# Performance work log

Hardware: AMD Instinct MI355X
Metric: run time of the kernel (lower is better)

The kernel has to match this reference:

```python
import jax, jax.numpy as jnp
import numpy as np

DM = 1024      # dmodel
HQK = 1024     # heads*dq == heads*dk == heads*dv
FF = 4096
VOCAB = 32000
NCAT = 75
DK = 64        # per-head dk used for 1/sqrt(dk) scaling
UNK_IDX = 1
EPS = 1e-5


def pos_encoding(n, dm):
    pos = jnp.arange(n, dtype=jnp.float32)[:, None]                  # [n,1]
    power = jnp.arange(0, dm, 2, dtype=jnp.float32) / dm             # [dm/2]
    denom = jnp.power(10000.0, power)                                # [dm/2]
    ang = pos / denom                                                # [n,dm/2]
    # even cols = sin, odd cols = cos (interleaved)
    return jnp.stack([jnp.sin(ang), jnp.cos(ang)], axis=-1).reshape(n, dm)


def layernorm(x, g, b):
    mu = jnp.mean(x, axis=-1, keepdims=True)
    var = jnp.var(x, axis=-1, keepdims=True)
    return (x - mu) * jax.lax.rsqrt(var + EPS) * g + b


def setup_inputs() -> dict:
    key = jax.random.key(0)
    ks = jax.random.split(key, 16)
    s = 0.02
    inp = {
        "input_indices": jax.random.randint(ks[0], (8, 2048), 0, VOCAB),
        "emb": jax.random.normal(ks[1], (VOCAB, DM), jnp.float32) * s,
        "Wq": jax.random.normal(ks[2], (DM, HQK), jnp.float32) * s,
        "bq": jnp.zeros((HQK,), jnp.float32),
        "Wk": jax.random.normal(ks[3], (DM, HQK), jnp.float32) * s,
        "bk": jnp.zeros((HQK,), jnp.float32),
        "Wv": jax.random.normal(ks[4], (DM, HQK), jnp.float32) * s,
        "bv": jnp.zeros((HQK,), jnp.float32),
        "Wu": jax.random.normal(ks[5], (HQK, DM), jnp.float32) * s,
        "bu": jnp.zeros((DM,), jnp.float32),
        "g1": jnp.ones((DM,), jnp.float32),
        "be1": jnp.zeros((DM,), jnp.float32),
        "W1": jax.random.normal(ks[6], (DM, FF), jnp.float32) * s,
        "b1": jnp.zeros((FF,), jnp.float32),
        "W2": jax.random.normal(ks[7], (FF, DM), jnp.float32) * s,
        "b2": jnp.zeros((DM,), jnp.float32),
        "g2": jnp.ones((DM,), jnp.float32),
        "be2": jnp.zeros((DM,), jnp.float32),
        "W3": jax.random.normal(ks[8], (DM, DM // 2), jnp.float32) * s,
        "b3": jnp.zeros((DM // 2,), jnp.float32),
        "W4": jax.random.normal(ks[9], (DM // 2, NCAT), jnp.float32) * s,
        "b4": jnp.zeros((NCAT,), jnp.float32),
        "g3": jnp.ones((NCAT,), jnp.float32),
        "be3": jnp.zeros((NCAT,), jnp.float32),
    }
    return inp


def reference(input_indices, emb, Wq, bq, Wk, bk, Wv, bv, Wu, bu, g1, be1,
              W1, b1, W2, b2, g2, be2, W3, b3, W4, b4, g3, be3):
    d, n = input_indices.shape
    idx = jnp.where(input_indices >= VOCAB, UNK_IDX, input_indices)
    x = emb[idx] + pos_encoding(n, DM)[None]                          # [d,n,dm]
    # attention WITHOUT softmax: scores = QK^T/sqrt(dk); attn = scores @ V
    q = x @ Wq + bq
    k = x @ Wk + bk
    v = x @ Wv + bv
    scores = jnp.einsum('bnd,bmd->bnm', q, k) / (DK ** 0.5)           # [d,n,n]
    attn = jnp.einsum('bnm,bmd->bnd', scores, v)                      # [d,n,hdv]
    u = attn @ Wu + bu
    h1 = layernorm(x + u, g1, be1)
    ffo = jax.nn.relu(h1 @ W1 + b1) @ W2 + b2
    h2 = layernorm(h1 + ffo, g2, be2)
    logits = jax.nn.relu(h2 @ W3 + b3) @ W4 + b4                      # [d,n,75]
    return jax.nn.sigmoid(layernorm(logits, g3, be3))
```

## Files before the change

### kernel.cpp

```cpp
#include <hip/hip_runtime.h>
#include <hip/hip_fp16.h>
#include <math.h>

#define DM    1024
#define FFD   4096
#define VOCAB 32000
#define NCAT  75
#define UNK_IDX 1
#define EPS   1e-5f
#define NB    8
#define SEQ   2048
#define T_TOK (NB*SEQ)

using u16   = unsigned short;
using half_t = _Float16;
using half8 = __attribute__((ext_vector_type(8))) _Float16;
using f32x4 = __attribute__((ext_vector_type(4))) float;

struct alignas(8) h4 { half_t s[4]; };

__device__ __forceinline__ void async16(const half_t* g, half_t* l) {
    __builtin_amdgcn_global_load_lds(
        (const __attribute__((address_space(1))) void*)g,
        (__attribute__((address_space(3))) void*)l,
        16, 0, 0);
}

__global__ __launch_bounds__(256)
void pe_kernel(float* __restrict__ pe)
{
    int gid = blockIdx.x * blockDim.x + threadIdx.x;
    if (gid >= SEQ * DM) return;
    int dcol = gid & (DM - 1);
    int t    = gid >> 10;
    int p = dcol >> 1;
    float power = (float)p / 512.0f;
    float denom = powf(10000.0f, power);
    float ang = (float)t / denom;
    pe[gid] = (dcol & 1) ? cosf(ang) : sinf(ang);
}

__global__ __launch_bounds__(256)
void embed_pos_kernel(const int* __restrict__ idx,
                      const float* __restrict__ emb,
                      const float* __restrict__ pe,
                      float* __restrict__ xf, half_t* __restrict__ xh)
{
    int gid4 = blockIdx.x * blockDim.x + threadIdx.x;
    if (gid4 >= T_TOK * DM / 4) return;
    int tok = gid4 >> 8;
    int c4  = (gid4 & 255) << 2;
    int t   = tok & (SEQ - 1);
    int id = idx[tok];
    if (id >= VOCAB || id < 0) id = UNK_IDX;
    float4 e = *(const float4*)(emb + (long long)id * DM + c4);
    float4 q = *(const float4*)(pe + (long long)t * DM + c4);
    float4 v = make_float4(e.x + q.x, e.y + q.y, e.z + q.z, e.w + q.w);
    *(float4*)(xf + (long long)tok * DM + c4) = v;
    h4 pk = {{(half_t)v.x, (half_t)v.y, (half_t)v.z, (half_t)v.w}};
    *(h4*)(xh + (long long)tok * DM + c4) = pk;
}

__global__ __launch_bounds__(256)
void transpose_h_kernel(const float* __restrict__ in, half_t* __restrict__ out,
                        int K, int N, int Npad)
{
    __shared__ float t[32][33];
    int n0 = blockIdx.x * 32, k0 = blockIdx.y * 32;
    int tx = threadIdx.x & 31, ty = threadIdx.x >> 5;
#pragma unroll
    for (int i = 0; i < 4; i++) {
        int k = k0 + ty + i * 8, n = n0 + tx;
        t[ty + i * 8][tx] = (k < K && n < N) ? in[(long long)k * N + n] : 0.f;
    }
    __syncthreads();
#pragma unroll
    for (int i = 0; i < 4; i++) {
        int n = n0 + ty + i * 8, k = k0 + tx;
        if (n < Npad && k < K)
            out[(long long)n * K + k] = (half_t)t[tx][ty + i * 8];
    }
}

__global__ __launch_bounds__(128)
void pad_bias_kernel(const float* __restrict__ b, float* __restrict__ bp)
{
    int i = threadIdx.x;
    bp[i] = (i < NCAT) ? b[i] : 0.f;
}

template<int OUT_MODE>
__global__ __launch_bounds__(256)
void gemm_nt(const half_t* __restrict__ A, const half_t* __restrict__ B,
             const float* __restrict__ bias, const float* __restrict__ resid,
             void* __restrict__ Cout,
             int M, int N, int K, int ld,
             long long sA, long long sB, long long sC,
             float scale, int do_relu)
{
    A += (long long)blockIdx.z * sA;
    B += (long long)blockIdx.z * sB;
    const int tid  = threadIdx.x;
    const int lane = tid & 63;
    const int w    = tid >> 6;
    const int wm   = w >> 1, wn = w & 1;
    const long long row0 = (long long)blockIdx.y * 128;
    const long long col0 = (long long)blockIdx.x * 128;

    __shared__ half_t smem[4 * 4096];
    half_t* const As = smem;
    half_t* const Bs = smem + 2 * 4096;

    f32x4 acc[4][4];
    const f32x4 zero = {0.f, 0.f, 0.f, 0.f};
#pragma unroll
    for (int i = 0; i < 4; i++)
#pragma unroll
        for (int j = 0; j < 4; j++) acc[i][j] = zero;

    const int ldrow = lane >> 2;
    const int swcol = (((lane & 3) << 3)) ^ ((ldrow & 3) << 3);
    const int fr    = lane & 15;
    const int kk8   = (lane >> 4) << 3;

    const int KT = K / 32;

#define ISSUE(k0, buf)                                                         \
    {                                                                          \
        _Pragma("unroll")                                                      \
        for (int it = 0; it < 2; ++it) {                                       \
            int rb = (it * 4 + w) * 16;                                        \
            long long ao = (row0 + rb + ldrow) * (long long)ld + (k0) + swcol; \
            long long bo = (col0 + rb + ldrow) * (long long)ld + (k0) + swcol; \
            async16(A + ao, As + (buf) * 4096 + rb * 32);                      \
            async16(B + bo, Bs + (buf) * 4096 + rb * 32);                      \
        }                                                                      \
    }

    ISSUE(0, 0);
    for (int kt = 0; kt < KT; ++kt) {
        const int cur = kt & 1;
        __syncthreads();
        if (kt + 1 < KT) ISSUE((kt + 1) * 32, cur ^ 1);

        half8 af[4], bf[4];
#pragma unroll
        for (int i = 0; i < 4; ++i) {
            int r   = wm * 64 + i * 16 + fr;
            int off = cur * 4096 + r * 32 + (kk8 ^ ((r & 3) << 3));
            af[i] = *(const half8*)(As + off);
        }
#pragma unroll
        for (int j = 0; j < 4; ++j) {
            int r   = wn * 64 + j * 16 + fr;
            int off = cur * 4096 + r * 32 + (kk8 ^ ((r & 3) << 3));
            bf[j] = *(const half8*)(Bs + off);
        }
#pragma unroll
        for (int i = 0; i < 4; ++i)
#pragma unroll
            for (int j = 0; j < 4; ++j)
                acc[i][j] = __builtin_amdgcn_mfma_f32_16x16x32_f16(
                    af[i], bf[j], acc[i][j], 0, 0, 0);
    }
#undef ISSUE

    float* ls = (float*)smem;
    const int ldp = 132;
    const int qr = (lane >> 4) * 4;
    const int lc = lane & 15;
    float bvj[4];
#pragma unroll
    for (int j = 0; j < 4; ++j)
        bvj[j] = bias ? bias[col0 + wn * 64 + j * 16 + lc] : 0.f;
    const float* rz = (OUT_MODE == 0 && resid) ? resid + (long long)blockIdx.z * sC : nullptr;

#pragma unroll
    for (int i = 0; i < 4; ++i) {
        __syncthreads();
#pragma unroll
        for (int j = 0; j < 4; ++j) {
            int col = wn * 64 + j * 16 + lc;
#pragma unroll
            for (int r = 0; r < 4; ++r) {
                float f = acc[i][j][r] * scale + bvj[j];
                if (do_relu) f = fmaxf(f, 0.f);
                ls[(wm * 16 + qr + r) * ldp + col] = f;
            }
        }
        __syncthreads();
        if (OUT_MODE == 2) {
#pragma unroll
            for (int rep = 0; rep < 4; ++rep) {
                int idx = rep * 256 + tid;
                int n   = idx >> 3;
                int k   = idx & 7;
                int lr0 = k * 4;
                h4 pk;
                long long arow0 = (lr0 < 16 ? 0 : 48) + i * 16 + lr0;
#pragma unroll
                for (int r = 0; r < 4; ++r)
                    pk.s[r] = (half_t)ls[(lr0 + r) * ldp + n];
                long long gr = row0 + arow0;
                int b  = (int)(gr >> 11);
                int tl = (int)(gr & (SEQ - 1));
                half_t* C = (half_t*)Cout;
                *(h4*)(C + (long long)b * N * SEQ + (col0 + n) * SEQ + tl) = pk;
            }
        } else {
#pragma unroll
            for (int rep = 0; rep < 4; ++rep) {
                int idx = rep * 256 + tid;
                int lr  = idx >> 5;
                int c4  = (idx & 31) << 2;
                long long arow = (lr < 16 ? 0 : 48) + i * 16 + lr;
                float4 v = *(float4*)&ls[lr * ldp + c4];
                long long base = (row0 + arow) * N + col0 + c4;
                if (OUT_MODE == 0) {
                    float* C = (float*)Cout + blockIdx.z * sC;
                    if (rz) {
                        float4 x = *(const float4*)(rz + base);
                        v.x += x.x; v.y += x.y; v.z += x.z; v.w += x.w;
                    }
                    *(float4*)(C + base) = v;
                } else {
                    half_t* C = (half_t*)Cout + blockIdx.z * sC;
                    h4 pk = {{(half_t)v.x, (half_t)v.y, (half_t)v.z, (half_t)v.w}};
                    *(h4*)(C + base) = pk;
                }
            }
        }
    }
}

__global__ __launch_bounds__(256)
void add_ln_kernel(const float* __restrict__ X, const float* __restrict__ Y,
                   const float* __restrict__ g, const float* __restrict__ b,
                   float* __restrict__ outf, half_t* __restrict__ outh)
{
    int row = blockIdx.x;
    int tid = threadIdx.x;
    float4 v = ((const float4*)(X + (long long)row * DM))[tid];
    if (Y) {
        float4 y = ((const float4*)(Y + (long long)row * DM))[tid];
        v.x += y.x; v.y += y.y; v.z += y.z; v.w += y.w;
    }
    float s  = v.x + v.y + v.z + v.w;
    float s2 = v.x * v.x + v.y * v.y + v.z * v.z + v.w * v.w;
#pragma unroll
    for (int o = 1; o < 64; o <<= 1) {
        s  += __shfl_xor(s,  o, 64);
        s2 += __shfl_xor(s2, o, 64);
    }
    __shared__ float rs[4], rs2[4], stats[2];
    int wid = tid >> 6;
    if ((tid & 63) == 0) { rs[wid] = s; rs2[wid] = s2; }
    __syncthreads();
    if (tid == 0) {
        float S  = rs[0] + rs[1] + rs[2] + rs[3];
        float S2 = rs2[0] + rs2[1] + rs2[2] + rs2[3];
        float mean = S / (float)DM;
        float var  = S2 / (float)DM - mean * mean;
        stats[0] = mean;
        stats[1] = rsqrtf(var + EPS);
    }
    __syncthreads();
    float mean = stats[0], rstd = stats[1];
    float4 gg = ((const float4*)g)[tid];
    float4 bb = ((const float4*)b)[tid];
    float4 o;
    o.x = (v.x - mean) * rstd * gg.x + bb.x;
    o.y = (v.y - mean) * rstd * gg.y + bb.y;
    o.z = (v.z - mean) * rstd * gg.z + bb.z;
    o.w = (v.w - mean) * rstd * gg.w + bb.w;
    if (outf) ((float4*)(outf + (long long)row * DM))[tid] = o;
    h4 pk = {{(half_t)o.x, (half_t)o.y, (half_t)o.z, (half_t)o.w}};
    *(h4*)(outh + (long long)row * DM + tid * 4) = pk;
}

__global__ __launch_bounds__(64)
void ln75_sigmoid_kernel(const float* __restrict__ L,
                         const float* __restrict__ g, const float* __restrict__ b,
                         float* __restrict__ out)
{
    int row = blockIdx.x;
    int t   = threadIdx.x;
    const float* lr = L + (long long)row * 128;
    float e0 = (t < NCAT) ? lr[t] : 0.f;
    float e1 = (t + 64 < NCAT) ? lr[t + 64] : 0.f;
    float s  = e0 + e1;
    float s2 = e0 * e0 + e1 * e1;
#pragma unroll
    for (int o = 1; o < 64; o <<= 1) {
        s  += __shfl_xor(s,  o, 64);
        s2 += __shfl_xor(s2, o, 64);
    }
    float mean = s / (float)NCAT;
    float var  = s2 / (float)NCAT - mean * mean;
    float rstd = rsqrtf(var + EPS);
    if (t < NCAT) {
        float z = (e0 - mean) * rstd * g[t] + b[t];
        out[(long long)row * NCAT + t] = 1.f / (1.f + expf(-z));
    }
    if (t + 64 < NCAT) {
        float z = (e1 - mean) * rstd * g[t + 64] + b[t + 64];
        out[(long long)row * NCAT + t + 64] = 1.f / (1.f + expf(-z));
    }
}

extern "C" void kernel_launch(void* const* d_in, const int* in_sizes, int n_in,
                              void* d_out, int out_size, void* d_ws, size_t ws_size,
                              hipStream_t stream)
{
    const int*   idx = (const int*)  d_in[0];
    const float* emb = (const float*)d_in[1];
    const float* Wq  = (const float*)d_in[2];
    const float* bq  = (const float*)d_in[3];
    const float* Wk  = (const float*)d_in[4];
    const float* bk  = (const float*)d_in[5];
    const float* Wv  = (const float*)d_in[6];
    const float* bv  = (const float*)d_in[7];
    const float* Wu  = (const float*)d_in[8];
    const float* bu  = (const float*)d_in[9];
    const float* g1  = (const float*)d_in[10];
    const float* be1 = (const float*)d_in[11];
    const float* W1  = (const float*)d_in[12];
    const float* b1  = (const float*)d_in[13];
    const float* W2  = (const float*)d_in[14];
    const float* b2  = (const float*)d_in[15];
    const float* g2  = (const float*)d_in[16];
    const float* be2 = (const float*)d_in[17];
    const float* W3  = (const float*)d_in[18];
    const float* b3  = (const float*)d_in[19];
    const float* W4  = (const float*)d_in[20];
    const float* b4  = (const float*)d_in[21];
    const float* g3  = (const float*)d_in[22];
    const float* be3 = (const float*)d_in[23];

    const long long TD  = (long long)T_TOK * DM;
    char* p = (char*)d_ws;
    char* R_A = p; p += TD * 4;
    char* R_B = p; p += TD * 2;
    char* R_C = p; p += TD * 2;
    char* R_D = p; p += TD * 2;
    char* R_D2 = p; p += TD * 2;
    char* R_E = p; p += TD * 4;
    char* R_F = p; p += (long long)NB * DM * DM * 4;
    char* R_G = p; p += (long long)T_TOK * 128 * 4;
    float* pe = (float*)p; p += (long long)SEQ * DM * 4;
    half_t* Wqh = (half_t*)p; p += DM*DM*2;
    half_t* Wkh = (half_t*)p; p += DM*DM*2;
    half_t* Wvh = (half_t*)p; p += DM*DM*2;
    half_t* Wuh = (half_t*)p; p += DM*DM*2;
    half_t* W1h = (half_t*)p; p += (long long)FFD*DM*2;
    half_t* W2h = (half_t*)p; p += (long long)DM*FFD*2;
    half_t* W3h = (half_t*)p; p += 512*DM*2;
    half_t* W4h = (half_t*)p; p += 128*512*2;
    float*  b4p = (float*)p;  p += 128*4;

    float*  Xf   = (float*)R_A;
    float*  ffo  = (float*)R_A;
    half_t* Xh   = (half_t*)R_B;
    half_t* h2h  = (half_t*)R_B;
    half_t* Qh   = (half_t*)R_C;
    half_t* h1h  = (half_t*)R_C;
    half_t* Kt   = (half_t*)R_D;
    half_t* Vt   = (half_t*)R_D2;
    half_t* f1h  = (half_t*)R_D;
    float*  usum = (float*)R_E;
    float*  h1f  = (float*)R_E;
    half_t* ktv2 = (half_t*)R_F;
    half_t* M2t  = (half_t*)(R_F + (long long)NB*DM*DM*2);
    half_t* l1h  = (half_t*)R_F;
    float*  LOG  = (float*)R_G;
    float*  out  = (float*)d_out;

    dim3 blk(256);

    transpose_h_kernel<<<dim3(32, 32),  blk, 0, stream>>>(Wq, Wqh, DM, DM, DM);
    transpose_h_kernel<<<dim3(32, 32),  blk, 0, stream>>>(Wk, Wkh, DM, DM, DM);
    transpose_h_kernel<<<dim3(32, 32),  blk, 0, stream>>>(Wv, Wvh, DM, DM, DM);
    transpose_h_kernel<<<dim3(32, 32),  blk, 0, stream>>>(Wu, Wuh, DM, DM, DM);
    transpose_h_kernel<<<dim3(128, 32), blk, 0, stream>>>(W1, W1h, DM, FFD, FFD);
    transpose_h_kernel<<<dim3(32, 128), blk, 0, stream>>>(W2, W2h, FFD, DM, DM);
    transpose_h_kernel<<<dim3(16, 32),  blk, 0, stream>>>(W3, W3h, DM, 512, 512);
    transpose_h_kernel<<<dim3(4, 16),   blk, 0, stream>>>(W4, W4h, 512, NCAT, 128);
    pad_bias_kernel<<<1, 128, 0, stream>>>(b4, b4p);
    pe_kernel<<<(SEQ * DM + 255) / 256, blk, 0, stream>>>(pe);

    embed_pos_kernel<<<(T_TOK * DM / 4 + 255) / 256, blk, 0, stream>>>(idx, emb, pe, Xf, Xh);

    gemm_nt<1><<<dim3(8, 128, 1), blk, 0, stream>>>(Xh, Wqh, bq, nullptr, Qh,
        T_TOK, DM, DM, DM, 0, 0, 0, 1.f, 0);
    gemm_nt<2><<<dim3(8, 128, 1), blk, 0, stream>>>(Xh, Wkh, bk, nullptr, Kt,
        T_TOK, DM, DM, DM, 0, 0, 0, 1.f, 0);
    gemm_nt<2><<<dim3(8, 128, 1), blk, 0, stream>>>(Xh, Wvh, bv, nullptr, Vt,
        T_TOK, DM, DM, DM, 0, 0, 0, 1.f, 0);

    gemm_nt<1><<<dim3(8, 8, NB), blk, 0, stream>>>(Kt, Vt, nullptr, nullptr, ktv2,
        DM, DM, SEQ, SEQ, (long long)DM * SEQ, (long long)DM * SEQ, (long long)DM * DM, 0.125f, 0);

    gemm_nt<1><<<dim3(8, 8, NB), blk, 0, stream>>>(Wuh, ktv2, nullptr, nullptr, M2t,
        DM, DM, DM, DM, 0, (long long)DM * DM, (long long)DM * DM, 1.f, 0);

    gemm_nt<0><<<dim3(8, 16, NB), blk, 0, stream>>>(Qh, M2t, bu, Xf, usum,
        SEQ, DM, DM, DM, (long long)SEQ * DM, (long long)DM * DM, (long long)SEQ * DM, 1.f, 0);

    add_ln_kernel<<<T_TOK, blk, 0, stream>>>(usum, nullptr, g1, be1, h1f, h1h);

    for (int c = 0; c < 2; c++) {
        const half_t* h1c  = h1h + (long long)c * 8192 * DM;
        float*        ffoc = ffo + (long long)c * 8192 * DM;
        gemm_nt<1><<<dim3(32, 64, 1), blk, 0, stream>>>(h1c, W1h, b1, nullptr, f1h,
            8192, FFD, DM, DM, 0, 0, 0, 1.f, 1);
        gemm_nt<0><<<dim3(8, 64, 1), blk, 0, stream>>>(f1h, W2h, b2, nullptr, ffoc,
            8192, DM, FFD, FFD, 0, 0, 0, 1.f, 0);
    }

    add_ln_kernel<<<T_TOK, blk, 0, stream>>>(h1f, ffo, g2, be2, nullptr, h2h);

    gemm_nt<1><<<dim3(4, 128, 1), blk, 0, stream>>>(h2h, W3h, b3, nullptr, l1h,
        T_TOK, 512, DM, DM, 0, 0, 0, 1.f, 1);
    gemm_nt<0><<<dim3(1, 128, 1), blk, 0, stream>>>(l1h, W4h, b4p, nullptr, LOG,
        T_TOK, 128, 512, 512, 0, 0, 0, 1.f, 0);

    ln75_sigmoid_kernel<<<T_TOK, 64, 0, stream>>>(LOG, g3, be3, out);
}
```

Measured before the change: 1.113 ms.

## Split-K the W2 GEMM, remap blocks across XCDs, fuse partial sum into LN

The gemm kernel gains a split-K dimension packed into blockIdx.z and an XCD-aware remapping of block indices, so consecutive tiles land on the same chiplet for better L2 reuse. The FFN down-projection now runs as a 2-way split-K producing two fp32 partials. The second layernorm runs per chunk and sums the residual, both partials and the bias. This raises occupancy for the 512-block W2 GEMM at the cost of an extra fp32 partial buffer write and read.

Result: slower. 1.136 ms (+2.1%).

```diff
diff --git a/kernel.cpp b/kernel.cpp
--- a/kernel.cpp
+++ b/kernel.cpp
@@ -96,16 +96,28 @@
              void* __restrict__ Cout,
              int M, int N, int K, int ld,
              long long sA, long long sB, long long sC,
+             long long sKA, long long sKB, long long sKC, int ksh,
              float scale, int do_relu)
 {
-    A += (long long)blockIdx.z * sA;
-    B += (long long)blockIdx.z * sB;
+    const int kz = (int)(blockIdx.z & ((1u << ksh) - 1u));
+    const int zb = (int)(blockIdx.z >> ksh);
+    A += (long long)zb * sA + (long long)kz * sKA;
+    B += (long long)zb * sB + (long long)kz * sKB;
+
+    const int nxy  = gridDim.x * gridDim.y;
+    const int orig = blockIdx.y * gridDim.x + blockIdx.x;
+    const int q = nxy >> 3, r = nxy & 7;
+    const int xcd = orig & 7, loc = orig >> 3;
+    const int wg  = (xcd < r ? xcd * (q + 1) : r * (q + 1) + (xcd - r) * q) + loc;
+    const int bx  = wg % gridDim.x;
+    const int by  = wg / gridDim.x;
+
     const int tid  = threadIdx.x;
     const int lane = tid & 63;
     const int w    = tid >> 6;
     const int wm   = w >> 1, wn = w & 1;
-    const long long row0 = (long long)blockIdx.y * 128;
-    const long long col0 = (long long)blockIdx.x * 128;
+    const long long row0 = (long long)by * 128;
+    const long long col0 = (long long)bx * 128;
 
     __shared__ half_t smem[4 * 4096];
     half_t* const As = smem;
@@ -173,7 +185,7 @@
 #pragma unroll
     for (int j = 0; j < 4; ++j)
         bvj[j] = bias ? bias[col0 + wn * 64 + j * 16 + lc] : 0.f;
-    const float* rz = (OUT_MODE == 0 && resid) ? resid + (long long)blockIdx.z * sC : nullptr;
+    const float* rz = (OUT_MODE == 0 && resid) ? resid + (long long)zb * sC : nullptr;
 
 #pragma unroll
     for (int i = 0; i < 4; ++i) {
@@ -217,14 +229,14 @@
                 float4 v = *(float4*)&ls[lr * ldp + c4];
                 long long base = (row0 + arow) * N + col0 + c4;
                 if (OUT_MODE == 0) {
-                    float* C = (float*)Cout + blockIdx.z * sC;
+                    float* C = (float*)Cout + (long long)zb * sC + (long long)kz * sKC;
                     if (rz) {
                         float4 x = *(const float4*)(rz + base);
                         v.x += x.x; v.y += x.y; v.z += x.z; v.w += x.w;
                     }
                     *(float4*)(C + base) = v;
                 } else {
-                    half_t* C = (half_t*)Cout + blockIdx.z * sC;
+                    half_t* C = (half_t*)Cout + (long long)zb * sC;
                     h4 pk = {{(half_t)v.x, (half_t)v.y, (half_t)v.z, (half_t)v.w}};
                     *(h4*)(C + base) = pk;
                 }
@@ -235,6 +247,7 @@
 
 __global__ __launch_bounds__(256)
 void add_ln_kernel(const float* __restrict__ X, const float* __restrict__ Y,
+                   const float* __restrict__ Z, const float* __restrict__ cb,
                    const float* __restrict__ g, const float* __restrict__ b,
                    float* __restrict__ outf, half_t* __restrict__ outh)
 {
@@ -244,6 +257,14 @@
     if (Y) {
         float4 y = ((const float4*)(Y + (long long)row * DM))[tid];
         v.x += y.x; v.y += y.y; v.z += y.z; v.w += y.w;
+    }
+    if (Z) {
+        float4 z = ((const float4*)(Z + (long long)row * DM))[tid];
+        v.x += z.x; v.y += z.y; v.z += z.z; v.w += z.w;
+    }
+    if (cb) {
+        float4 c = ((const float4*)cb)[tid];
+        v.x += c.x; v.y += c.y; v.z += c.z; v.w += c.w;
     }
     float s  = v.x + v.y + v.z + v.w;
     float s2 = v.x * v.x + v.y * v.y + v.z * v.z + v.w * v.w;
@@ -359,7 +380,7 @@
     float*  b4p = (float*)p;  p += 128*4;
 
     float*  Xf   = (float*)R_A;
-    float*  ffo  = (float*)R_A;
+    float*  Pff  = (float*)R_A;
     half_t* Xh   = (half_t*)R_B;
     half_t* h2h  = (half_t*)R_B;
     half_t* Qh   = (half_t*)R_C;
@@ -391,38 +412,43 @@
     embed_pos_kernel<<<(T_TOK * DM / 4 + 255) / 256, blk, 0, stream>>>(idx, emb, pe, Xf, Xh);
 
     gemm_nt<1><<<dim3(8, 128, 1), blk, 0, stream>>>(Xh, Wqh, bq, nullptr, Qh,
-        T_TOK, DM, DM, DM, 0, 0, 0, 1.f, 0);
+        T_TOK, DM, DM, DM, 0, 0, 0, 0, 0, 0, 0, 1.f, 0);
     gemm_nt<2><<<dim3(8, 128, 1), blk, 0, stream>>>(Xh, Wkh, bk, nullptr, Kt,
-        T_TOK, DM, DM, DM, 0, 0, 0, 1.f, 0);
+        T_TOK, DM, DM, DM, 0, 0, 0, 0, 0, 0, 0, 1.f, 0);
     gemm_nt<2><<<dim3(8, 128, 1), blk, 0, stream>>>(Xh, Wvh, bv, nullptr, Vt,
-        T_TOK, DM, DM, DM, 0, 0, 0, 1.f, 0);
+        T_TOK, DM, DM, DM, 0, 0, 0, 0, 0, 0, 0, 1.f, 0);
 
     gemm_nt<1><<<dim3(8, 8, NB), blk, 0, stream>>>(Kt, Vt, nullptr, nullptr, ktv2,
-        DM, DM, SEQ, SEQ, (long long)DM * SEQ, (long long)DM * SEQ, (long long)DM * DM, 0.125f, 0);
+        DM, DM, SEQ, SEQ, (long long)DM * SEQ, (long long)DM * SEQ, (long long)DM * DM,
+        0, 0, 0, 0, 0.125f, 0);
 
     gemm_nt<1><<<dim3(8, 8, NB), blk, 0, stream>>>(Wuh, ktv2, nullptr, nullptr, M2t,
-        DM, DM, DM, DM, 0, (long long)DM * DM, (long long)DM * DM, 1.f, 0);
+        DM, DM, DM, DM, 0, (long long)DM * DM, (long long)DM * DM,
+        0, 0, 0, 0, 1.f, 0);
 
     gemm_nt<0><<<dim3(8, 16, NB), blk, 0, stream>>>(Qh, M2t, bu, Xf, usum,
-        SEQ, DM, DM, DM, (long long)SEQ * DM, (long long)DM * DM, (long long)SEQ * DM, 1.f, 0);
-
-    add_ln_kernel<<<T_TOK, blk, 0, stream>>>(usum, nullptr, g1, be1, h1f, h1h);
+        SEQ, DM, DM, DM, (long long)SEQ * DM, (long long)DM * DM, (long long)SEQ * DM,
+        0, 0, 0, 0, 1.f, 0);
+
+    add_ln_kernel<<<T_TOK, blk, 0, stream>>>(usum, nullptr, nullptr, nullptr,
+                                             g1, be1, h1f, h1h);
 
     for (int c = 0; c < 2; c++) {
-        const half_t* h1c  = h1h + (long long)c * 8192 * DM;
-        float*        ffoc = ffo + (long long)c * 8192 * DM;
+        const half_t* h1c = h1h + (long long)c * 8192 * DM;
         gemm_nt<1><<<dim3(32, 64, 1), blk, 0, stream>>>(h1c, W1h, b1, nullptr, f1h,
-            8192, FFD, DM, DM, 0, 0, 0, 1.f, 1);
-        gemm_nt<0><<<dim3(8, 64, 1), blk, 0, stream>>>(f1h, W2h, b2, nullptr, ffoc,
-            8192, DM, FFD, FFD, 0, 0, 0, 1.f, 0);
-    }
-
-    add_ln_kernel<<<T_TOK, blk, 0, stream>>>(h1f, ffo, g2, be2, nullptr, h2h);
+            8192, FFD, DM, DM, 0, 0, 0, 0, 0, 0, 0, 1.f, 1);
+        gemm_nt<0><<<dim3(8, 64, 2), blk, 0, stream>>>(f1h, W2h, nullptr, nullptr, Pff,
+            8192, DM, 2048, FFD, 0, 0, 0,
+            2048, 2048, (long long)8192 * DM, 1, 1.f, 0);
+        add_ln_kernel<<<8192, blk, 0, stream>>>(h1f + (long long)c * 8192 * DM,
+            Pff, Pff + (long long)8192 * DM, b2, g2, be2,
+            nullptr, h2h + (long long)c * 8192 * DM);
+    }
 
     gemm_nt<1><<<dim3(4, 128, 1), blk, 0, stream>>>(h2h, W3h, b3, nullptr, l1h,
-        T_TOK, 512, DM, DM, 0, 0, 0, 1.f, 1);
+        T_TOK, 512, DM, DM, 0, 0, 0, 0, 0, 0, 0, 1.f, 1);
     gemm_nt<0><<<dim3(1, 128, 1), blk, 0, stream>>>(l1h, W4h, b4p, nullptr, LOG,
-        T_TOK, 128, 512, 512, 0, 0, 0, 1.f, 0);
+        T_TOK, 128, 512, 512, 0, 0, 0, 0, 0, 0, 0, 1.f, 0);
 
     ln75_sigmoid_kernel<<<T_TOK, 64, 0, stream>>>(LOG, g3, be3, out);
 }
```

## Add 256x256 MFMA GEMM kernel with split-K for FFN and fuse LN reduction

Applied to the files above, without the earlier changes.

Adds a new 512-thread GEMM with 256x256 tiles, double-buffered async global-to-LDS loads, interleaved MFMA phases and XCD-aware block remapping. It replaces the Q projection, the attention output, W1 and W2 GEMMs. W2 now runs as split-K over two halves, and the partial sums plus b2 are added inside the layernorm kernel. The larger tiles aim at more data reuse and higher MFMA utilization, at the cost of heavier register and LDS use and an extra partial buffer write for the split-K path.

Result: faster. 1.007 ms (-9.5%).

```diff
diff --git a/kernel.cpp b/kernel.cpp
--- a/kernel.cpp
+++ b/kernel.cpp
@@ -25,6 +25,13 @@
         (__attribute__((address_space(3))) void*)l,
         16, 0, 0);
 }
+
+#define VMW(n) asm volatile("s_waitcnt vmcnt(" #n ")" ::: "memory")
+#define LGKM0()                                            \
+    do {                                                   \
+        asm volatile("s_waitcnt lgkmcnt(0)" ::: "memory"); \
+        __builtin_amdgcn_sched_barrier(0);                 \
+    } while (0)
 
 __global__ __launch_bounds__(256)
 void pe_kernel(float* __restrict__ pe)
@@ -233,8 +240,181 @@
     }
 }
 
+template<int OUT_MODE>
+__global__ __launch_bounds__(512, 2)
+void gemm256(const half_t* __restrict__ A, const half_t* __restrict__ B,
+             const float* __restrict__ bias, const float* __restrict__ resid,
+             void* __restrict__ Cout,
+             int N, int K, int ld,
+             long long sA, long long sB, long long sC,
+             long long sKA, long long sKB, long long sKC, int ksh,
+             float scale, int do_relu)
+{
+    const int kz       = (int)(blockIdx.z & ((1u << ksh) - 1u));
+    const long long zb = (long long)(blockIdx.z >> ksh);
+    A += zb * sA + (long long)kz * sKA;
+    B += zb * sB + (long long)kz * sKB;
+
+    int bx = blockIdx.x, by = blockIdx.y;
+    const int nxy = gridDim.x * gridDim.y;
+    if ((nxy & 7) == 0) {
+        const int orig = by * gridDim.x + bx;
+        const int cpx  = nxy >> 3;
+        const int wg   = (orig & 7) * cpx + (orig >> 3);
+        bx = wg % gridDim.x;
+        by = wg / gridDim.x;
+    }
+    const long long row0 = (long long)by * 256;
+    const long long col0 = (long long)bx * 256;
+
+    const int tid  = threadIdx.x;
+    const int lane = tid & 63;
+    const int w    = tid >> 6;
+    const int wm   = w >> 2, wn = w & 3;
+    const int fr   = lane & 15;
+    const int kk8  = (lane >> 4) << 3;
+
+    __shared__ half_t smem[65536];
+    half_t* const As = smem;
+    half_t* const Bs = smem + 32768;
+
+    f32x4 acc[8][4];
+    const f32x4 zero = {0.f, 0.f, 0.f, 0.f};
+#pragma unroll
+    for (int i = 0; i < 8; i++)
+#pragma unroll
+        for (int j = 0; j < 4; j++) acc[i][j] = zero;
+
+    const int srow = w * 16 + (lane >> 2);
+    const int scol = (lane & 3) << 3;
+
+#define STAGE(G, plane, rb, kb)                                                   \
+    {                                                                             \
+        _Pragma("unroll")                                                         \
+        for (int it_ = 0; it_ < 2; ++it_) {                                       \
+            async16((G) + ((rb) + it_ * 128 + srow) * (long long)ld + (kb) + scol,\
+                    (plane) + it_ * 4096 + w * 512);                              \
+        }                                                                         \
+    }
+#define RDA(base_, roff_)                                                         \
+    _Pragma("unroll")                                                             \
+    for (int q_ = 0; q_ < 4; ++q_)                                                \
+        af[q_] = *(const half8*)((base_) + ((roff_) + q_ * 16 + fr) * 32 + kk8);
+#define RDB(base_)                                                                \
+    _Pragma("unroll")                                                             \
+    for (int q_ = 0; q_ < 4; ++q_)                                                \
+        bf[q_] = *(const half8*)((base_) + (wn * 64 + q_ * 16 + fr) * 32 + kk8);
+#define MM16(o_)                                                                  \
+    _Pragma("unroll")                                                             \
+    for (int mi_ = 0; mi_ < 4; ++mi_)                                             \
+    _Pragma("unroll")                                                             \
+    for (int ni_ = 0; ni_ < 4; ++ni_)                                             \
+        acc[(o_) + mi_][ni_] = __builtin_amdgcn_mfma_f32_16x16x32_f16(            \
+            af[mi_], bf[ni_], acc[(o_) + mi_][ni_], 0, 0, 0);
+#define MFMA_PHASE(o_)                                      \
+    __builtin_amdgcn_s_barrier();                           \
+    LGKM0();                                                \
+    __builtin_amdgcn_s_setprio(1);                          \
+    MM16(o_);                                               \
+    __builtin_amdgcn_s_setprio(0);                          \
+    __builtin_amdgcn_s_barrier();
+
+    const int KT = K >> 6;
+
+    STAGE(A, As,        row0, 0);
+    STAGE(B, Bs,        col0, 0);
+    STAGE(A, As + 8192, row0, 32);
+    STAGE(B, Bs + 8192, col0, 32);
+    VMW(4);
+    __builtin_amdgcn_s_barrier();
+
+    half8 af[4], bf[4];
+    for (int t = 0; t < KT; ++t) {
+        const int db = (t & 1) << 14;
+        const int nb = 16384 - db;
+        const half_t* Ap0 = As + db;
+        const half_t* Ap1 = As + db + 8192;
+        const half_t* Bp0 = Bs + db;
+        const half_t* Bp1 = Bs + db + 8192;
+        const int kn = (t + 1 < KT ? t + 1 : t) << 6;
+
+        RDA(Ap0, wm * 128); RDB(Bp0);
+        STAGE(A, As + nb, row0, kn);
+        MFMA_PHASE(0);
+        RDA(Ap0, wm * 128 + 64);
+        STAGE(B, Bs + nb, col0, kn);
+        VMW(4);
+        MFMA_PHASE(4);
+        RDA(Ap1, wm * 128); RDB(Bp1);
+        STAGE(A, As + nb + 8192, row0, kn + 32);
+        MFMA_PHASE(0);
+        RDA(Ap1, wm * 128 + 64);
+        STAGE(B, Bs + nb + 8192, col0, kn + 32);
+        VMW(4);
+        MFMA_PHASE(4);
+    }
+#undef STAGE
+#undef RDA
+#undef RDB
+#undef MM16
+#undef MFMA_PHASE
+
+    VMW(0);
+    __syncthreads();
+    float* const ls = (float*)smem;
+    const int ldp = 268;
+    const int qr = (lane >> 4) * 4;
+    const int lc = lane & 15;
+    float bvn[4];
+#pragma unroll
+    for (int ni = 0; ni < 4; ++ni)
+        bvn[ni] = bias ? bias[col0 + wn * 64 + ni * 16 + lc] : 0.f;
+    const float* rz = (OUT_MODE == 0 && resid) ? resid + zb * sC : nullptr;
+
+#pragma unroll
+    for (int i = 0; i < 4; ++i) {
+        if (i) __syncthreads();
+#pragma unroll
+        for (int h = 0; h < 2; ++h) {
+            const int mi = 2 * i + h;
+#pragma unroll
+            for (int ni = 0; ni < 4; ++ni) {
+#pragma unroll
+                for (int r = 0; r < 4; ++r) {
+                    float f = acc[mi][ni][r] * scale + bvn[ni];
+                    if (do_relu) f = fmaxf(f, 0.f);
+                    ls[(wm * 32 + h * 16 + qr + r) * ldp + wn * 64 + ni * 16 + lc] = f;
+                }
+            }
+        }
+        __syncthreads();
+#pragma unroll
+        for (int rep = 0; rep < 8; ++rep) {
+            int idx2 = rep * 512 + tid;
+            int r  = idx2 >> 6;
+            int c4 = (idx2 & 63) << 2;
+            long long grow = row0 + (r < 32 ? i * 32 + r : 128 + i * 32 + (r - 32));
+            long long base = grow * N + col0 + c4;
+            float4 v = *(float4*)&ls[r * ldp + c4];
+            if (OUT_MODE == 0) {
+                float* C = (float*)Cout + zb * sC + (long long)kz * sKC;
+                if (rz) {
+                    float4 x = *(const float4*)(rz + base);
+                    v.x += x.x; v.y += x.y; v.z += x.z; v.w += x.w;
+                }
+                *(float4*)(C + base) = v;
+            } else {
+                half_t* C = (half_t*)Cout + zb * sC;
+                h4 pk = {{(half_t)v.x, (half_t)v.y, (half_t)v.z, (half_t)v.w}};
+                *(h4*)(C + base) = pk;
+            }
+        }
+    }
+}
+
 __global__ __launch_bounds__(256)
 void add_ln_kernel(const float* __restrict__ X, const float* __restrict__ Y,
+                   const float* __restrict__ Z, const float* __restrict__ cb,
                    const float* __restrict__ g, const float* __restrict__ b,
                    float* __restrict__ outf, half_t* __restrict__ outh)
 {
@@ -244,6 +424,14 @@
     if (Y) {
         float4 y = ((const float4*)(Y + (long long)row * DM))[tid];
         v.x += y.x; v.y += y.y; v.z += y.z; v.w += y.w;
+    }
+    if (Z) {
+        float4 z = ((const float4*)(Z + (long long)row * DM))[tid];
+        v.x += z.x; v.y += z.y; v.z += z.z; v.w += z.w;
+    }
+    if (cb) {
+        float4 c = ((const float4*)cb)[tid];
+        v.x += c.x; v.y += c.y; v.z += c.z; v.w += c.w;
     }
     float s  = v.x + v.y + v.z + v.w;
     float s2 = v.x * v.x + v.y * v.y + v.z * v.z + v.w * v.w;
@@ -359,7 +547,7 @@
     float*  b4p = (float*)p;  p += 128*4;
 
     float*  Xf   = (float*)R_A;
-    float*  ffo  = (float*)R_A;
+    float*  Pff  = (float*)R_A;
     half_t* Xh   = (half_t*)R_B;
     half_t* h2h  = (half_t*)R_B;
     half_t* Qh   = (half_t*)R_C;
@@ -376,6 +564,7 @@
     float*  out  = (float*)d_out;
 
     dim3 blk(256);
+    dim3 blk5(512);
 
     transpose_h_kernel<<<dim3(32, 32),  blk, 0, stream>>>(Wq, Wqh, DM, DM, DM);
     transpose_h_kernel<<<dim3(32, 32),  blk, 0, stream>>>(Wk, Wkh, DM, DM, DM);
@@ -390,34 +579,38 @@
 
     embed_pos_kernel<<<(T_TOK * DM / 4 + 255) / 256, blk, 0, stream>>>(idx, emb, pe, Xf, Xh);
 
-    gemm_nt<1><<<dim3(8, 128, 1), blk, 0, stream>>>(Xh, Wqh, bq, nullptr, Qh,
-        T_TOK, DM, DM, DM, 0, 0, 0, 1.f, 0);
+    gemm256<1><<<dim3(4, 64, 1), blk5, 0, stream>>>(Xh, Wqh, bq, nullptr, Qh,
+        DM, DM, DM, 0, 0, 0, 0, 0, 0, 0, 1.f, 0);
     gemm_nt<2><<<dim3(8, 128, 1), blk, 0, stream>>>(Xh, Wkh, bk, nullptr, Kt,
         T_TOK, DM, DM, DM, 0, 0, 0, 1.f, 0);
     gemm_nt<2><<<dim3(8, 128, 1), blk, 0, stream>>>(Xh, Wvh, bv, nullptr, Vt,
         T_TOK, DM, DM, DM, 0, 0, 0, 1.f, 0);
 
     gemm_nt<1><<<dim3(8, 8, NB), blk, 0, stream>>>(Kt, Vt, nullptr, nullptr, ktv2,
-        DM, DM, SEQ, SEQ, (long long)DM * SEQ, (long long)DM * SEQ, (long long)DM * DM, 0.125f, 0);
+        DM, DM, SEQ, SEQ, (long long)DM * SEQ, (long long)DM * SEQ, (long long)DM * DM,
+        0.125f, 0);
 
     gemm_nt<1><<<dim3(8, 8, NB), blk, 0, stream>>>(Wuh, ktv2, nullptr, nullptr, M2t,
         DM, DM, DM, DM, 0, (long long)DM * DM, (long long)DM * DM, 1.f, 0);
 
-    gemm_nt<0><<<dim3(8, 16, NB), blk, 0, stream>>>(Qh, M2t, bu, Xf, usum,
-        SEQ, DM, DM, DM, (long long)SEQ * DM, (long long)DM * DM, (long long)SEQ * DM, 1.f, 0);
-
-    add_ln_kernel<<<T_TOK, blk, 0, stream>>>(usum, nullptr, g1, be1, h1f, h1h);
+    gemm256<0><<<dim3(4, 8, NB), blk5, 0, stream>>>(Qh, M2t, bu, Xf, usum,
+        DM, DM, DM, (long long)SEQ * DM, (long long)DM * DM, (long long)SEQ * DM,
+        0, 0, 0, 0, 1.f, 0);
+
+    add_ln_kernel<<<T_TOK, blk, 0, stream>>>(usum, nullptr, nullptr, nullptr,
+                                             g1, be1, h1f, h1h);
 
     for (int c = 0; c < 2; c++) {
-        const half_t* h1c  = h1h + (long long)c * 8192 * DM;
-        float*        ffoc = ffo + (long long)c * 8192 * DM;
-        gemm_nt<1><<<dim3(32, 64, 1), blk, 0, stream>>>(h1c, W1h, b1, nullptr, f1h,
-            8192, FFD, DM, DM, 0, 0, 0, 1.f, 1);
-        gemm_nt<0><<<dim3(8, 64, 1), blk, 0, stream>>>(f1h, W2h, b2, nullptr, ffoc,
-            8192, DM, FFD, FFD, 0, 0, 0, 1.f, 0);
-    }
-
-    add_ln_kernel<<<T_TOK, blk, 0, stream>>>(h1f, ffo, g2, be2, nullptr, h2h);
+        const half_t* h1c = h1h + (long long)c * 8192 * DM;
+        gemm256<1><<<dim3(16, 32, 1), blk5, 0, stream>>>(h1c, W1h, b1, nullptr, f1h,
+            FFD, DM, DM, 0, 0, 0, 0, 0, 0, 0, 1.f, 1);
+        gemm256<0><<<dim3(4, 32, 2), blk5, 0, stream>>>(f1h, W2h, nullptr, nullptr, Pff,
+            DM, 2048, FFD, 0, 0, 0,
+            2048, 2048, (long long)8192 * DM, 1, 1.f, 0);
+        add_ln_kernel<<<8192, blk, 0, stream>>>(h1f + (long long)c * 8192 * DM,
+            Pff, Pff + (long long)8192 * DM, b2, g2, be2,
+            nullptr, h2h + (long long)c * 8192 * DM);
+    }
 
     gemm_nt<1><<<dim3(4, 128, 1), blk, 0, stream>>>(h2h, W3h, b3, nullptr, l1h,
         T_TOK, 512, DM, DM, 0, 0, 0, 1.f, 1);
```
